# Kernel optimization log

Measured on AMD Instinct MI355X. Metric: run time of the kernel, lower is better.

Reference implementation:

```python
import jax, jax.numpy as jnp
import numpy as np

N_ATOMS = 1048576
N_CRYS = 8192
NFEA = 128
NCLS = 5
LN_EPS = 1e-5


def setup_inputs() -> dict:
    key = jax.random.key(0)
    k1, k2, k3 = jax.random.split(key, 3)
    data_crys_fea = jax.random.normal(k1, (N_ATOMS, NFEA), dtype=jnp.float32)
    # Contiguous non-empty [start, end) ranges partitioning [0, N_ATOMS)
    rng = np.random.default_rng(0)
    cuts = np.sort(rng.choice(np.arange(1, N_ATOMS), size=N_CRYS - 1, replace=False))
    starts = np.concatenate([[0], cuts])
    ends = np.concatenate([cuts, [N_ATOMS]])
    data_crys_idx = jnp.asarray(np.stack([starts, ends], axis=1).astype(np.int32))
    ln_weight = jnp.ones((NFEA,), dtype=jnp.float32)
    ln_bias = jnp.zeros((NFEA,), dtype=jnp.float32)
    out_w = jax.random.normal(k2, (NCLS, NFEA), dtype=jnp.float32) / np.sqrt(NFEA).astype(np.float32)
    out_b = jax.random.normal(k3, (NCLS,), dtype=jnp.float32) * 0.01
    return {
        "data_crys_fea": data_crys_fea,
        "data_crys_idx": data_crys_idx,
        "ln_weight": ln_weight,
        "ln_bias": ln_bias,
        "out_w": out_w,
        "out_b": out_b,
    }


def reference(data_crys_fea, data_crys_idx, ln_weight, ln_bias, out_w, out_b):
    # --- pool: per-crystal mean over contiguous [start, end) atom ranges ---
    starts = data_crys_idx[:, 0]
    ends = data_crys_idx[:, 1]
    n_atoms = data_crys_fea.shape[0]
    # segment id of each atom via searchsorted on sorted starts
    seg = jnp.searchsorted(starts, jnp.arange(n_atoms, dtype=starts.dtype), side="right") - 1
    seg_sum = jax.ops.segment_sum(data_crys_fea, seg, num_segments=N_CRYS)  # [n_crys, F]
    lens = (ends - starts).astype(data_crys_fea.dtype)
    pooled = seg_sum / lens[:, None]
    # --- LayerNorm over features (biased variance, eps=1e-5, like torch) ---
    mu = jnp.mean(pooled, axis=-1, keepdims=True)
    var = jnp.var(pooled, axis=-1, keepdims=True)
    normed = (pooled - mu) / jnp.sqrt(var + LN_EPS) * ln_weight + ln_bias
    # --- Softplus then Linear ---
    act = jax.nn.softplus(normed)  # [n_crys, F]
    my_output = act @ out_w.T + out_b  # [n_crys, n_cls]
    return my_output, act
```

## Files before the change

kernel.cpp:

```cpp
#include <hip/hip_runtime.h>
#include <hip/hip_bf16.h>

#define NFEA 128
#define NCLS 5
#define LN_EPS 1e-5f

__global__ __launch_bounds__(256) void crys_fea_kernel(
    const float* __restrict__ fea,
    const int2*  __restrict__ idx,
    const float* __restrict__ lnw,
    const float* __restrict__ lnb,
    const float* __restrict__ outw,
    const float* __restrict__ outb,
    float* __restrict__ out_cls,
    float* __restrict__ out_act)
{
    const int c = blockIdx.x;
    const int2 se = idx[c];
    const int start = se.x;
    const int end   = se.y;
    const int len   = end - start;

    const int tid = threadIdx.x;
    const int fc  = tid & 31;
    const int al  = tid >> 5;

    float4 acc = make_float4(0.f, 0.f, 0.f, 0.f);
    const float4* __restrict__ fea4 = (const float4*)fea;
    for (int a = start + al; a < end; a += 8) {
        float4 v = fea4[(size_t)a * 32 + fc];
        acc.x += v.x; acc.y += v.y; acc.z += v.z; acc.w += v.w;
    }

    __shared__ float4 red4[8][32];
    red4[al][fc] = acc;
    __syncthreads();

    __shared__ float pooled[NFEA];
    __shared__ float s_mu, s_rstd;

    if (tid < NFEA) {
        const float* redf = (const float*)red4;
        float s = 0.f;
        #pragma unroll
        for (int g = 0; g < 8; ++g) s += redf[g * NFEA + tid];
        pooled[tid] = s / (float)len;
    }
    __syncthreads();

    if (tid < 64) {
        float v = pooled[tid] + pooled[tid + 64];
        #pragma unroll
        for (int off = 32; off; off >>= 1) v += __shfl_down(v, off);
        if (tid == 0) s_mu = v * (1.f / NFEA);
    }
    __syncthreads();
    if (tid < 64) {
        const float mu = s_mu;
        const float d0 = pooled[tid] - mu;
        const float d1 = pooled[tid + 64] - mu;
        float v = d0 * d0 + d1 * d1;
        #pragma unroll
        for (int off = 32; off; off >>= 1) v += __shfl_down(v, off);
        if (tid == 0) s_rstd = rsqrtf(v * (1.f / NFEA) + LN_EPS);
    }
    __syncthreads();

    __shared__ float s_act[NFEA];
    if (tid < NFEA) {
        const float x = (pooled[tid] - s_mu) * s_rstd * lnw[tid] + lnb[tid];
        const float a = (x > 0.f) ? (x + log1pf(expf(-x))) : log1pf(expf(x));
        s_act[tid] = a;
        out_act[(size_t)c * NFEA + tid] = a;
    }
    __syncthreads();

    if (tid < 64) {
        const float a0 = s_act[tid];
        const float a1 = s_act[tid + 64];
        #pragma unroll
        for (int k = 0; k < NCLS; ++k) {
            float p = a0 * outw[k * NFEA + tid] + a1 * outw[k * NFEA + tid + 64];
            #pragma unroll
            for (int off = 32; off; off >>= 1) p += __shfl_down(p, off);
            if (tid == 0) out_cls[(size_t)c * NCLS + k] = p + outb[k];
        }
    }
}

extern "C" void kernel_launch(void* const* d_in, const int* in_sizes, int n_in,
                              void* d_out, int out_size, void* d_ws, size_t ws_size,
                              hipStream_t stream) {
    const float* fea  = (const float*)d_in[0];
    const int2*  idx  = (const int2*)d_in[1];
    const float* lnw  = (const float*)d_in[2];
    const float* lnb  = (const float*)d_in[3];
    const float* outw = (const float*)d_in[4];
    const float* outb = (const float*)d_in[5];

    const int n_crys = in_sizes[1] / 2;

    float* out_cls = (float*)d_out;
    float* out_act = (float*)d_out + (size_t)n_crys * NCLS;

    crys_fea_kernel<<<n_crys, 256, 0, stream>>>(
        fea, idx, lnw, lnb, outw, outb, out_cls, out_act);
}
```

Measured before the change: 144.7 us.

## Split pooling into atom-chunked partial sums with atomics plus finalize kernel

```diff
diff --git a/kernel.cpp b/kernel.cpp
--- a/kernel.cpp
+++ b/kernel.cpp
@@ -4,9 +4,66 @@
 #define NFEA 128
 #define NCLS 5
 #define LN_EPS 1e-5f
+#define CHUNK 128
 
-__global__ __launch_bounds__(256) void crys_fea_kernel(
+__global__ __launch_bounds__(256) void seg_partial_kernel(
     const float* __restrict__ fea,
+    const int2*  __restrict__ idx,
+    float* __restrict__ seg_sum,
+    int n_crys)
+{
+    const int a0 = blockIdx.x * CHUNK;
+    const int a1 = a0 + CHUNK;
+
+    int lo = 0, hi = n_crys - 1;
+    while (lo < hi) {
+        int mid = (lo + hi + 1) >> 1;
+        if (idx[mid].x <= a0) lo = mid; else hi = mid - 1;
+    }
+    int s = lo;
+
+    const int tid = threadIdx.x;
+    const int fc  = tid & 31;
+    const int al  = tid >> 5;
+
+    const float4* __restrict__ fea4 = (const float4*)fea;
+    __shared__ float4 red4[8][32];
+
+    int rs = a0;
+    while (rs < a1) {
+        const int re = min(idx[s].y, a1);
+
+        float4 acc0 = make_float4(0.f, 0.f, 0.f, 0.f);
+        float4 acc1 = make_float4(0.f, 0.f, 0.f, 0.f);
+        int a = rs + al;
+        for (; a + 8 < re; a += 16) {
+            float4 v0 = fea4[(size_t)a * 32 + fc];
+            float4 v1 = fea4[(size_t)(a + 8) * 32 + fc];
+            acc0.x += v0.x; acc0.y += v0.y; acc0.z += v0.z; acc0.w += v0.w;
+            acc1.x += v1.x; acc1.y += v1.y; acc1.z += v1.z; acc1.w += v1.w;
+        }
+        if (a < re) {
+            float4 v = fea4[(size_t)a * 32 + fc];
+            acc0.x += v.x; acc0.y += v.y; acc0.z += v.z; acc0.w += v.w;
+        }
+        acc0.x += acc1.x; acc0.y += acc1.y; acc0.z += acc1.z; acc0.w += acc1.w;
+
+        red4[al][fc] = acc0;
+        __syncthreads();
+        if (tid < NFEA) {
+            const float* redf = (const float*)red4;
+            float ssum = 0.f;
+            #pragma unroll
+            for (int g = 0; g < 8; ++g) ssum += redf[g * NFEA + tid];
+            atomicAdd(&seg_sum[(size_t)s * NFEA + tid], ssum);
+        }
+        __syncthreads();
+        rs = re; ++s;
+    }
+}
+
+__global__ __launch_bounds__(64) void finalize_kernel(
+    const float* __restrict__ seg_sum,
     const int2*  __restrict__ idx,
     const float* __restrict__ lnw,
     const float* __restrict__ lnb,
@@ -15,76 +72,39 @@
     float* __restrict__ out_cls,
     float* __restrict__ out_act)
 {
-    const int c = blockIdx.x;
+    const int c   = blockIdx.x;
+    const int tid = threadIdx.x;
     const int2 se = idx[c];
-    const int start = se.x;
-    const int end   = se.y;
-    const int len   = end - start;
+    const float inv_len = 1.f / (float)(se.y - se.x);
 
-    const int tid = threadIdx.x;
-    const int fc  = tid & 31;
-    const int al  = tid >> 5;
+    float p0 = seg_sum[(size_t)c * NFEA + tid]      * inv_len;
+    float p1 = seg_sum[(size_t)c * NFEA + tid + 64] * inv_len;
 
-    float4 acc = make_float4(0.f, 0.f, 0.f, 0.f);
-    const float4* __restrict__ fea4 = (const float4*)fea;
-    for (int a = start + al; a < end; a += 8) {
-        float4 v = fea4[(size_t)a * 32 + fc];
-        acc.x += v.x; acc.y += v.y; acc.z += v.z; acc.w += v.w;
-    }
+    float t = p0 + p1;
+    #pragma unroll
+    for (int off = 32; off; off >>= 1) t += __shfl_xor(t, off);
+    const float mu = t * (1.f / NFEA);
 
-    __shared__ float4 red4[8][32];
-    red4[al][fc] = acc;
-    __syncthreads();
+    const float d0 = p0 - mu, d1 = p1 - mu;
+    float v = d0 * d0 + d1 * d1;
+    #pragma unroll
+    for (int off = 32; off; off >>= 1) v += __shfl_xor(v, off);
+    const float rstd = rsqrtf(v * (1.f / NFEA) + LN_EPS);
 
-    __shared__ float pooled[NFEA];
-    __shared__ float s_mu, s_rstd;
+    const float x0 = d0 * rstd * lnw[tid]      + lnb[tid];
+    const float x1 = d1 * rstd * lnw[tid + 64] + lnb[tid + 64];
+    const float a0 = (x0 > 0.f) ? x0 + log1pf(expf(-x0)) : log1pf(expf(x0));
+    const float a1 = (x1 > 0.f) ? x1 + log1pf(expf(-x1)) : log1pf(expf(x1));
 
-    if (tid < NFEA) {
-        const float* redf = (const float*)red4;
-        float s = 0.f;
+    out_act[(size_t)c * NFEA + tid]      = a0;
+    out_act[(size_t)c * NFEA + tid + 64] = a1;
+
+    #pragma unroll
+    for (int k = 0; k < NCLS; ++k) {
+        float p = a0 * outw[k * NFEA + tid] + a1 * outw[k * NFEA + tid + 64];
         #pragma unroll
-        for (int g = 0; g < 8; ++g) s += redf[g * NFEA + tid];
-        pooled[tid] = s / (float)len;
-    }
-    __syncthreads();
-
-    if (tid < 64) {
-        float v = pooled[tid] + pooled[tid + 64];
-        #pragma unroll
-        for (int off = 32; off; off >>= 1) v += __shfl_down(v, off);
-        if (tid == 0) s_mu = v * (1.f / NFEA);
-    }
-    __syncthreads();
-    if (tid < 64) {
-        const float mu = s_mu;
-        const float d0 = pooled[tid] - mu;
-        const float d1 = pooled[tid + 64] - mu;
-        float v = d0 * d0 + d1 * d1;
-        #pragma unroll
-        for (int off = 32; off; off >>= 1) v += __shfl_down(v, off);
-        if (tid == 0) s_rstd = rsqrtf(v * (1.f / NFEA) + LN_EPS);
-    }
-    __syncthreads();
-
-    __shared__ float s_act[NFEA];
-    if (tid < NFEA) {
-        const float x = (pooled[tid] - s_mu) * s_rstd * lnw[tid] + lnb[tid];
-        const float a = (x > 0.f) ? (x + log1pf(expf(-x))) : log1pf(expf(x));
-        s_act[tid] = a;
-        out_act[(size_t)c * NFEA + tid] = a;
-    }
-    __syncthreads();
-
-    if (tid < 64) {
-        const float a0 = s_act[tid];
-        const float a1 = s_act[tid + 64];
-        #pragma unroll
-        for (int k = 0; k < NCLS; ++k) {
-            float p = a0 * outw[k * NFEA + tid] + a1 * outw[k * NFEA + tid + 64];
-            #pragma unroll
-            for (int off = 32; off; off >>= 1) p += __shfl_down(p, off);
-            if (tid == 0) out_cls[(size_t)c * NCLS + k] = p + outb[k];
-        }
+        for (int off = 32; off; off >>= 1) p += __shfl_xor(p, off);
+        if (tid == k) out_cls[(size_t)c * NCLS + k] = p + outb[k];
     }
 }
 
@@ -98,11 +118,16 @@
     const float* outw = (const float*)d_in[4];
     const float* outb = (const float*)d_in[5];
 
-    const int n_crys = in_sizes[1] / 2;
+    const int n_crys  = in_sizes[1] / 2;
+    const int n_atoms = in_sizes[0] / NFEA;
 
+    float* seg_sum = (float*)d_ws;
     float* out_cls = (float*)d_out;
     float* out_act = (float*)d_out + (size_t)n_crys * NCLS;
 
-    crys_fea_kernel<<<n_crys, 256, 0, stream>>>(
-        fea, idx, lnw, lnb, outw, outb, out_cls, out_act);
+    hipMemsetAsync(seg_sum, 0, (size_t)n_crys * NFEA * sizeof(float), stream);
+
+    seg_partial_kernel<<<n_atoms / CHUNK, 256, 0, stream>>>(fea, idx, seg_sum, n_crys);
+    finalize_kernel<<<n_crys, 64, 0, stream>>>(seg_sum, idx, lnw, lnb, outw, outb,
+                                               out_cls, out_act);
 }
```

Result: faster. 123.9 us (median of 2 runs) (-14.3%).
